# Optimization experiments

Hardware: AMD Instinct MI355X
Metric: run time of the kernel (lower is better)

The kernel has to match this reference:

```python
import jax, jax.numpy as jnp
import numpy as np

# --- constants from config ---
CU, CV, F, BASE = 257.446, 197.718, 387.777, 0.239965
INLIER_THRESHOLD = 0.5
ERROR_TOLERANCE = 0.5   # '3D'
NUM_ITERATIONS = 256
DIM = '3D'
BATCH, NPTS, NSAMP = 64, 16384, 6


def se3_inv(T):
    # T: ...x4x4 SE(3); inverse = [R^T, -R^T t]
    R = T[..., :3, :3]
    t = T[..., :3, 3:4]
    Rt = jnp.swapaxes(R, -1, -2)
    top = jnp.concatenate([Rt, -Rt @ t], axis=-1)
    bottom = jnp.broadcast_to(jnp.array([0.0, 0.0, 0.0, 1.0], T.dtype), top.shape[:-2] + (1, 4))
    return jnp.concatenate([top, bottom], axis=-2)


def weighted_svd_transform(src, trg, w):
    # src, trg: Bx4xS homogeneous points; w: Bx1xS weights. Returns T_trg_src (Bx4x4).
    ps, pt = src[:, :3, :], trg[:, :3, :]
    w_sum = jnp.sum(w, axis=2, keepdims=True)
    cs = jnp.sum(ps * w, axis=2, keepdims=True) / w_sum  # Bx3x1
    ct = jnp.sum(pt * w, axis=2, keepdims=True) / w_sum
    qs, qt = ps - cs, pt - ct
    cov = jnp.einsum('bis,bjs->bij', qt * w, qs)  # Bx3x3
    U, _, Vt = jnp.linalg.svd(cov)
    det = jnp.linalg.det(U @ Vt)
    diag = jnp.stack([jnp.ones_like(det), jnp.ones_like(det), det], axis=-1)  # Bx3
    R = jnp.einsum('bij,bj,bjk->bik', U, diag, Vt)
    t = ct - R @ cs
    top = jnp.concatenate([R, t], axis=2)
    bottom = jnp.broadcast_to(jnp.array([0.0, 0.0, 0.0, 1.0], src.dtype), (src.shape[0], 1, 4))
    return jnp.concatenate([top, bottom], axis=1)


def stereo_project(pts):
    # pts: Bx4xN homogeneous camera-frame points -> Bx4xN stereo image coords (ul, vl, ur, vr)
    M = jnp.array([[F, 0.0, CU, 0.0],
                   [0.0, F, CV, 0.0],
                   [F, 0.0, CU, -F * BASE],
                   [0.0, F, CV, 0.0]], pts.dtype)
    z = pts[:, 2:3, :]
    return jnp.einsum('ij,bjn->bin', M, pts) / z


def setup_inputs() -> dict:
    key = jax.random.key(0)
    ks = jax.random.split(key, 6)
    def homog(k):
        p = jax.random.normal(k, (BATCH, 3, NPTS), jnp.float32) * 5.0
        p = p.at[:, 2, :].set(jnp.abs(p[:, 2, :]) + 1.0)  # positive depth
        return jnp.concatenate([p, jnp.ones((BATCH, 1, NPTS), jnp.float32)], axis=1)
    keypoints_3D_src = homog(ks[0])
    keypoints_3D_trg = homog(ks[1])
    keypoints_2D_trg = jax.random.uniform(ks[2], (BATCH, 2, NPTS), jnp.float32) * 512.0
    valid_pts_src = jax.random.randint(ks[3], (BATCH, 1, NPTS), 0, 2).astype(jnp.int32)
    valid_pts_trg = jax.random.randint(ks[4], (BATCH, 1, NPTS), 0, 2).astype(jnp.int32)
    weights = jax.random.uniform(ks[5], (BATCH, 1, NPTS), jnp.float32, 1e-3, 1.0)
    # vehicle->sensor transform: small rotation about x + translation
    c, s = np.cos(0.1), np.sin(0.1)
    T_s_v = jnp.array([[1, 0, 0, 0.2], [0, c, -s, 0.0], [0, s, c, 1.0], [0, 0, 0, 1]], jnp.float32)
    return {'keypoints_3D_src': keypoints_3D_src, 'keypoints_3D_trg': keypoints_3D_trg,
            'keypoints_2D_trg': keypoints_2D_trg, 'valid_pts_src': valid_pts_src,
            'valid_pts_trg': valid_pts_trg, 'weights': weights, 'T_s_v': T_s_v}


def reference(keypoints_3D_src, keypoints_3D_trg, keypoints_2D_trg,
              valid_pts_src, valid_pts_trg, weights, T_s_v):
    B, _, N = keypoints_3D_src.shape
    pts_src = jax.lax.stop_gradient(keypoints_3D_src)
    pts_trg = jax.lax.stop_gradient(keypoints_3D_trg)
    pts2_trg = jax.lax.stop_gradient(keypoints_2D_trg)
    w = jax.lax.stop_gradient(weights)
    valid = (valid_pts_src[:, 0, :] > 0) & (valid_pts_trg[:, 0, :] > 0)  # BxN
    T_s_v_b = jnp.broadcast_to(T_s_v, (B, 4, 4))
    T_v_s_b = se3_inv(T_s_v_b)

    rand_idx = jax.random.randint(jax.random.key(42), (NUM_ITERATIONS, B, NSAMP), 0, N)

    def body(carry, idx):
        max_inl, inliers = carry
        idx4 = idx[:, None, :]
        s_src = jnp.take_along_axis(pts_src, jnp.broadcast_to(idx4, (B, 4, NSAMP)), axis=2)
        s_trg = jnp.take_along_axis(pts_trg, jnp.broadcast_to(idx4, (B, 4, NSAMP)), axis=2)
        s_w = jnp.take_along_axis(w, idx4, axis=2)
        T_trg_src = weighted_svd_transform(s_src, s_trg, s_w)          # Bx4x4
        T_cam = T_s_v_b @ T_trg_src @ T_v_s_b                          # Bx4x4
        est_3D = jnp.einsum('bij,bjn->bin', T_cam, pts_src)            # Bx4xN
        if DIM == '2D':
            est_2D = stereo_project(est_3D)[:, 0:2, :]
            err = jnp.linalg.norm(pts2_trg - est_2D, axis=1)
        else:
            err = jnp.linalg.norm(pts_trg[:, 0:3, :] - est_3D[:, 0:3, :], axis=1)
        small = (err < ERROR_TOLERANCE) & valid                        # BxN
        num = jnp.sum(small, axis=1).astype(jnp.int32)                 # B
        better = num > max_inl
        inliers = jnp.where(better[:, None], small, inliers)
        max_inl = jnp.where(better, num, max_inl)
        return (max_inl, inliers), None

    init = (jnp.zeros((B,), jnp.int32), jnp.zeros((B, N), bool))
    (_, inliers), _ = jax.lax.scan(body, init, rand_idx)
    return inliers.astype(jnp.float32)
```

## Files before the change

### kernel.cpp

```cpp
#include <hip/hip_runtime.h>
#include <stdint.h>
#include <math.h>

#define NPTS   16384
#define NBATCH 64
#define NITER  256
#define NSAMP  6
#define PPT    16
#define NCHUNK 4
#define ISPLIT 8
#define IPB    (NITER / ISPLIT)

__device__ __forceinline__ uint32_t rotl32(uint32_t v, uint32_t r) {
  return (v << r) | (v >> (32u - r));
}
__device__ __forceinline__ void tf_round(uint32_t& x0, uint32_t& x1, uint32_t r) {
  x0 += x1; x1 = rotl32(x1, r); x1 ^= x0;
}
__device__ void threefry2x32(uint32_t k0, uint32_t k1, uint32_t x0, uint32_t x1,
                             uint32_t& o0, uint32_t& o1) {
  uint32_t ks2 = k0 ^ k1 ^ 0x1BD11BDAu;
  x0 += k0; x1 += k1;
  tf_round(x0,x1,13); tf_round(x0,x1,15); tf_round(x0,x1,26); tf_round(x0,x1,6);
  x0 += k1; x1 += ks2 + 1u;
  tf_round(x0,x1,17); tf_round(x0,x1,29); tf_round(x0,x1,16); tf_round(x0,x1,24);
  x0 += ks2; x1 += k0 + 2u;
  tf_round(x0,x1,13); tf_round(x0,x1,15); tf_round(x0,x1,26); tf_round(x0,x1,6);
  x0 += k0; x1 += k1 + 3u;
  tf_round(x0,x1,17); tf_round(x0,x1,29); tf_round(x0,x1,16); tf_round(x0,x1,24);
  x0 += k1; x1 += ks2 + 4u;
  tf_round(x0,x1,13); tf_round(x0,x1,15); tf_round(x0,x1,26); tf_round(x0,x1,6);
  x0 += ks2; x1 += k0 + 5u;
  o0 = x0; o1 = x1;
}

template<int P, int Q>
__device__ __forceinline__ void jrot(double S[3][3], double V[3][3]) {
  double apq = S[P][Q];
  if (fabs(apq) > 1e-300) {
    double tau = (S[Q][Q] - S[P][P]) / (2.0 * apq);
    double t = copysign(1.0, tau) / (fabs(tau) + sqrt(1.0 + tau * tau));
    double c = 1.0 / sqrt(1.0 + t * t);
    double sn = t * c;
    #pragma unroll
    for (int k = 0; k < 3; ++k) {
      double skp = S[k][P], skq = S[k][Q];
      S[k][P] = c * skp - sn * skq;
      S[k][Q] = sn * skp + c * skq;
    }
    #pragma unroll
    for (int k = 0; k < 3; ++k) {
      double spk = S[P][k], sqk = S[Q][k];
      S[P][k] = c * spk - sn * sqk;
      S[Q][k] = sn * spk + c * sqk;
    }
    #pragma unroll
    for (int k = 0; k < 3; ++k) {
      double vkp = V[k][P], vkq = V[k][Q];
      V[k][P] = c * vkp - sn * vkq;
      V[k][Q] = sn * vkp + c * vkq;
    }
  }
}

__device__ __forceinline__ void swapd(double& a, double& b) { double t=a; a=b; b=t; }

__global__ __launch_bounds__(64) void fit_kernel(
    const float* __restrict__ src, const float* __restrict__ trg,
    const float* __restrict__ wts, const float* __restrict__ Tsv,
    float* __restrict__ models ,
    int* __restrict__ counts ) {
  const int b = blockIdx.x >> 2;
  const int iter = ((blockIdx.x & 3) << 6) | threadIdx.x;

  counts[b * NITER + iter] = 0;

  uint32_t K0, K1;
  threefry2x32(0u, 42u, 0u, 1u, K0, K1);

  const uint32_t base = (uint32_t)((iter * NBATCH + b) * NSAMP);
  int idx[NSAMP];
  #pragma unroll
  for (int s = 0; s < NSAMP; ++s) {
    uint32_t y0, y1;
    threefry2x32(K0, K1, 0u, base + (uint32_t)s, y0, y1);
    idx[s] = (int)((y0 ^ y1) & (uint32_t)(NPTS - 1));
  }

  const float* sb = src + (size_t)b * 4 * NPTS;
  const float* tb = trg + (size_t)b * 4 * NPTS;
  const float* wb = wts + (size_t)b * NPTS;

  float px[NSAMP], py[NSAMP], pz[NSAMP], qx[NSAMP], qy[NSAMP], qz[NSAMP], wv[NSAMP];
  #pragma unroll
  for (int s = 0; s < NSAMP; ++s) {
    int j = idx[s];
    px[s] = sb[j]; py[s] = sb[NPTS + j]; pz[s] = sb[2 * NPTS + j];
    qx[s] = tb[j]; qy[s] = tb[NPTS + j]; qz[s] = tb[2 * NPTS + j];
    wv[s] = wb[j];
  }

  double wsum = 0, csx = 0, csy = 0, csz = 0, ctx = 0, cty = 0, ctz = 0;
  #pragma unroll
  for (int s = 0; s < NSAMP; ++s) {
    double w = (double)wv[s];
    wsum += w;
    csx += (double)px[s] * w; csy += (double)py[s] * w; csz += (double)pz[s] * w;
    ctx += (double)qx[s] * w; cty += (double)qy[s] * w; ctz += (double)qz[s] * w;
  }
  double iw = 1.0 / wsum;
  csx *= iw; csy *= iw; csz *= iw; ctx *= iw; cty *= iw; ctz *= iw;

  double C00=0,C01=0,C02=0,C10=0,C11=0,C12=0,C20=0,C21=0,C22=0;
  #pragma unroll
  for (int s = 0; s < NSAMP; ++s) {
    double w = (double)wv[s];
    double ax = ((double)qx[s]-ctx)*w, ay = ((double)qy[s]-cty)*w, az = ((double)qz[s]-ctz)*w;
    double bx = (double)px[s]-csx, by = (double)py[s]-csy, bz = (double)pz[s]-csz;
    C00 += ax*bx; C01 += ax*by; C02 += ax*bz;
    C10 += ay*bx; C11 += ay*by; C12 += ay*bz;
    C20 += az*bx; C21 += az*by; C22 += az*bz;
  }

  double S[3][3], V[3][3] = {{1,0,0},{0,1,0},{0,0,1}};
  S[0][0] = C00*C00 + C10*C10 + C20*C20;
  S[0][1] = C00*C01 + C10*C11 + C20*C21;
  S[0][2] = C00*C02 + C10*C12 + C20*C22;
  S[1][1] = C01*C01 + C11*C11 + C21*C21;
  S[1][2] = C01*C02 + C11*C12 + C21*C22;
  S[2][2] = C02*C02 + C12*C12 + C22*C22;
  S[1][0] = S[0][1]; S[2][0] = S[0][2]; S[2][1] = S[1][2];
  #pragma unroll 1
  for (int sweep = 0; sweep < 6; ++sweep) {
    jrot<0,1>(S, V); jrot<0,2>(S, V); jrot<1,2>(S, V);
  }

  double l0 = S[0][0], l1 = S[1][1], l2 = S[2][2];
  double v0x=V[0][0], v0y=V[1][0], v0z=V[2][0];
  double v1x=V[0][1], v1y=V[1][1], v1z=V[2][1];
  double v2x=V[0][2], v2y=V[1][2], v2z=V[2][2];
  if (l0 < l1) { swapd(l0,l1); swapd(v0x,v1x); swapd(v0y,v1y); swapd(v0z,v1z); }
  if (l1 < l2) { swapd(l1,l2); swapd(v1x,v2x); swapd(v1y,v2y); swapd(v1z,v2z); }
  if (l0 < l1) { swapd(l0,l1); swapd(v0x,v1x); swapd(v0y,v1y); swapd(v0z,v1z); }

  double u0x = C00*v0x + C01*v0y + C02*v0z;
  double u0y = C10*v0x + C11*v0y + C12*v0z;
  double u0z = C20*v0x + C21*v0y + C22*v0z;
  double n0 = sqrt(u0x*u0x + u0y*u0y + u0z*u0z);
  double r0 = (n0 > 1e-150) ? 1.0 / n0 : 0.0;
  u0x *= r0; u0y *= r0; u0z *= r0;
  double u1x = C00*v1x + C01*v1y + C02*v1z;
  double u1y = C10*v1x + C11*v1y + C12*v1z;
  double u1z = C20*v1x + C21*v1y + C22*v1z;
  double d01 = u1x*u0x + u1y*u0y + u1z*u0z;
  u1x -= d01*u0x; u1y -= d01*u0y; u1z -= d01*u0z;
  double n1 = sqrt(u1x*u1x + u1y*u1y + u1z*u1z);
  double r1 = (n1 > 1e-150) ? 1.0 / n1 : 0.0;
  u1x *= r1; u1y *= r1; u1z *= r1;
  double u2x = u0y*u1z - u0z*u1y;
  double u2y = u0z*u1x - u0x*u1z;
  double u2z = u0x*u1y - u0y*u1x;
  double detV = v0x*(v1y*v2z - v1z*v2y) - v0y*(v1x*v2z - v1z*v2x) + v0z*(v1x*v2y - v1y*v2x);
  double R00 = u0x*v0x + u1x*v1x + detV*u2x*v2x;
  double R01 = u0x*v0y + u1x*v1y + detV*u2x*v2y;
  double R02 = u0x*v0z + u1x*v1z + detV*u2x*v2z;
  double R10 = u0y*v0x + u1y*v1x + detV*u2y*v2x;
  double R11 = u0y*v0y + u1y*v1y + detV*u2y*v2y;
  double R12 = u0y*v0z + u1y*v1z + detV*u2y*v2z;
  double R20 = u0z*v0x + u1z*v1x + detV*u2z*v2x;
  double R21 = u0z*v0y + u1z*v1y + detV*u2z*v2y;
  double R22 = u0z*v0z + u1z*v1z + detV*u2z*v2z;
  double tx = ctx - (R00*csx + R01*csy + R02*csz);
  double ty = cty - (R10*csx + R11*csy + R12*csz);
  double tz = ctz - (R20*csx + R21*csy + R22*csz);

  double A[4][4];
  #pragma unroll
  for (int i = 0; i < 4; ++i)
    #pragma unroll
    for (int j = 0; j < 4; ++j) A[i][j] = (double)Tsv[i*4 + j];
  double Tts[4][4] = {{R00,R01,R02,tx},{R10,R11,R12,ty},{R20,R21,R22,tz},{0,0,0,1}};
  double I[4][4];
  I[0][0]=A[0][0]; I[0][1]=A[1][0]; I[0][2]=A[2][0];
  I[1][0]=A[0][1]; I[1][1]=A[1][1]; I[1][2]=A[2][1];
  I[2][0]=A[0][2]; I[2][1]=A[1][2]; I[2][2]=A[2][2];
  I[0][3] = -(I[0][0]*A[0][3] + I[0][1]*A[1][3] + I[0][2]*A[2][3]);
  I[1][3] = -(I[1][0]*A[0][3] + I[1][1]*A[1][3] + I[1][2]*A[2][3]);
  I[2][3] = -(I[2][0]*A[0][3] + I[2][1]*A[1][3] + I[2][2]*A[2][3]);
  I[3][0]=0; I[3][1]=0; I[3][2]=0; I[3][3]=1;
  double M1[4][4];
  #pragma unroll
  for (int i = 0; i < 4; ++i)
    #pragma unroll
    for (int j = 0; j < 4; ++j)
      M1[i][j] = A[i][0]*Tts[0][j] + A[i][1]*Tts[1][j] + A[i][2]*Tts[2][j] + A[i][3]*Tts[3][j];
  float* mo = models + ((size_t)b * NITER + iter) * 12;
  #pragma unroll
  for (int i = 0; i < 3; ++i)
    #pragma unroll
    for (int j = 0; j < 4; ++j)
      mo[i*4 + j] = (float)(M1[i][0]*I[0][j] + M1[i][1]*I[1][j] + M1[i][2]*I[2][j] + M1[i][3]*I[3][j]);
}

__global__ __launch_bounds__(256) void count_kernel(
    const float* __restrict__ src, const float* __restrict__ trg,
    const int* __restrict__ vs, const int* __restrict__ vt,
    const float* __restrict__ models, int* __restrict__ counts) {
  __shared__ float4 M4[IPB * 3];
  __shared__ int cl[IPB];
  const int b      = blockIdx.x >> 5;
  const int isplit = (blockIdx.x >> 2) & (ISPLIT - 1);
  const int chunk  = blockIdx.x & (NCHUNK - 1);
  const int ibase  = isplit * IPB;

  const float4* mb4 = (const float4*)(models + ((size_t)b * NITER + ibase) * 12);
  for (int i = threadIdx.x; i < IPB * 3; i += 256) M4[i] = mb4[i];
  if (threadIdx.x < IPB) cl[threadIdx.x] = 0;
  __syncthreads();

  const float* sb = src + (size_t)b * 4 * NPTS;
  const float* tb = trg + (size_t)b * 4 * NPTS;
  const int* vsb = vs + (size_t)b * NPTS;
  const int* vtb = vt + (size_t)b * NPTS;
  const int p0 = chunk * (256 * PPT) + threadIdx.x;

  float sx[PPT], sy[PPT], sz[PPT], tx[PPT], ty[PPT], tz[PPT];
  #pragma unroll
  for (int k = 0; k < PPT; ++k) {
    int p = p0 + k * 256;
    bool vd = (vsb[p] > 0) && (vtb[p] > 0);
    sx[k] = sb[p]; sy[k] = sb[NPTS + p]; sz[k] = sb[2 * NPTS + p];
    tx[k] = vd ? tb[p] : 3.0e38f;
    ty[k] = tb[NPTS + p]; tz[k] = tb[2 * NPTS + p];
  }

  for (int it = 0; it < IPB; it += 2) {
    float4 r0 = M4[it * 3 + 0], r1 = M4[it * 3 + 1], r2 = M4[it * 3 + 2];
    int c0 = 0;
    #pragma unroll
    for (int k = 0; k < PPT; ++k) {
      float ex = fmaf(r0.x, sx[k], fmaf(r0.y, sy[k], fmaf(r0.z, sz[k], r0.w)));
      float ey = fmaf(r1.x, sx[k], fmaf(r1.y, sy[k], fmaf(r1.z, sz[k], r1.w)));
      float ez = fmaf(r2.x, sx[k], fmaf(r2.y, sy[k], fmaf(r2.z, sz[k], r2.w)));
      float dx = tx[k] - ex, dy = ty[k] - ey, dz = tz[k] - ez;
      float e2 = fmaf(dx, dx, fmaf(dy, dy, dz * dz));
      c0 += (e2 < 0.25f) ? 1 : 0;
    }
    float4 q0 = M4[it * 3 + 3], q1 = M4[it * 3 + 4], q2 = M4[it * 3 + 5];
    int c1 = 0;
    #pragma unroll
    for (int k = 0; k < PPT; ++k) {
      float ex = fmaf(q0.x, sx[k], fmaf(q0.y, sy[k], fmaf(q0.z, sz[k], q0.w)));
      float ey = fmaf(q1.x, sx[k], fmaf(q1.y, sy[k], fmaf(q1.z, sz[k], q1.w)));
      float ez = fmaf(q2.x, sx[k], fmaf(q2.y, sy[k], fmaf(q2.z, sz[k], q2.w)));
      float dx = tx[k] - ex, dy = ty[k] - ey, dz = tz[k] - ez;
      float e2 = fmaf(dx, dx, fmaf(dy, dy, dz * dz));
      c1 += (e2 < 0.25f) ? 1 : 0;
    }
    unsigned s = (unsigned)c0 | ((unsigned)c1 << 16);
    s += __shfl_xor(s, 32); s += __shfl_xor(s, 16); s += __shfl_xor(s, 8);
    s += __shfl_xor(s, 4);  s += __shfl_xor(s, 2);  s += __shfl_xor(s, 1);
    const int lane = threadIdx.x & 63;
    if (lane == 0)      atomicAdd(&cl[it],     (int)(s & 0xffffu));
    else if (lane == 1) atomicAdd(&cl[it + 1], (int)(s >> 16));
  }
  __syncthreads();
  if (threadIdx.x < IPB)
    atomicAdd(&counts[(size_t)b * NITER + ibase + threadIdx.x], cl[threadIdx.x]);
}

__global__ __launch_bounds__(256) void output_kernel(
    const float* __restrict__ src, const float* __restrict__ trg,
    const int* __restrict__ vs, const int* __restrict__ vt,
    const float* __restrict__ models, const int* __restrict__ counts,
    float* __restrict__ out) {
  const int tid = blockIdx.x * 256 + threadIdx.x;
  const int b = tid >> 14;
  const int p = tid & (NPTS - 1);

  __shared__ int sbest[4];
  {
    int c = counts[b * NITER + threadIdx.x];
    int key = (c << 8) | (NITER - 1 - threadIdx.x);
    key = max(key, __shfl_xor(key, 32));
    key = max(key, __shfl_xor(key, 16));
    key = max(key, __shfl_xor(key, 8));
    key = max(key, __shfl_xor(key, 4));
    key = max(key, __shfl_xor(key, 2));
    key = max(key, __shfl_xor(key, 1));
    if ((threadIdx.x & 63) == 0) sbest[threadIdx.x >> 6] = key;
  }
  __syncthreads();
  const int best = max(max(sbest[0], sbest[1]), max(sbest[2], sbest[3]));
  const int it = (NITER - 1) - (best & 255);

  const float* m = models + ((size_t)b * NITER + it) * 12;
  float m00=m[0], m01=m[1], m02=m[2],  m03=m[3];
  float m10=m[4], m11=m[5], m12=m[6],  m13=m[7];
  float m20=m[8], m21=m[9], m22=m[10], m23=m[11];
  const float* sb = src + (size_t)b * 4 * NPTS;
  const float* tb = trg + (size_t)b * 4 * NPTS;
  float sxv = sb[p], syv = sb[NPTS + p], szv = sb[2 * NPTS + p];
  float txv = tb[p], tyv = tb[NPTS + p], tzv = tb[2 * NPTS + p];
  bool v = (vs[(size_t)b * NPTS + p] > 0) && (vt[(size_t)b * NPTS + p] > 0);
  float ex = fmaf(m00, sxv, fmaf(m01, syv, fmaf(m02, szv, m03)));
  float ey = fmaf(m10, sxv, fmaf(m11, syv, fmaf(m12, szv, m13)));
  float ez = fmaf(m20, sxv, fmaf(m21, syv, fmaf(m22, szv, m23)));
  float dx = txv - ex, dy = tyv - ey, dz = tzv - ez;
  float e2 = fmaf(dx, dx, fmaf(dy, dy, dz * dz));
  out[tid] = (e2 < 0.25f && v) ? 1.0f : 0.0f;
}

extern "C" void kernel_launch(void* const* d_in, const int* in_sizes, int n_in,
                              void* d_out, int out_size, void* d_ws, size_t ws_size,
                              hipStream_t stream) {
  (void)in_sizes; (void)n_in; (void)out_size; (void)ws_size;
  const float* src = (const float*)d_in[0];
  const float* trg = (const float*)d_in[1];
  const int*   vs  = (const int*)d_in[3];
  const int*   vt  = (const int*)d_in[4];
  const float* wts = (const float*)d_in[5];
  const float* Tsv = (const float*)d_in[6];
  float* out = (float*)d_out;

  char* ws = (char*)d_ws;
  float* models = (float*)ws;
  int* counts   = (int*)(ws + (size_t)NBATCH * NITER * 12 * 4);

  fit_kernel<<<NBATCH * 4, 64, 0, stream>>>(src, trg, wts, Tsv, models, counts);
  count_kernel<<<NBATCH * ISPLIT * NCHUNK, 256, 0, stream>>>(src, trg, vs, vt, models, counts);
  output_kernel<<<(NBATCH * NPTS) / 256, 256, 0, stream>>>(src, trg, vs, vt, models, counts, out);
}
```

Measured before the change: 216.9 us.

## Vectorize point loads, read models via scalar loads, drop shared-memory staging in count kernel

The count kernel now gives each thread a contiguous run of 16 points and loads them with float4/int4 vector loads instead of strided scalar loads. Model matrices are read straight from global memory as wave-uniform values (likely scalar loads) instead of being staged in LDS behind a barrier. Per-wave counts go straight to global atomics instead of block-local LDS atomics, and launch bounds now request 3 blocks per SIMD. This trades LDS traffic and the barrier for more global atomics and a possible rise in register pressure.

```diff
diff --git a/kernel.cpp b/kernel.cpp
--- a/kernel.cpp
+++ b/kernel.cpp
@@ -202,57 +202,68 @@
       mo[i*4 + j] = (float)(M1[i][0]*I[0][j] + M1[i][1]*I[1][j] + M1[i][2]*I[2][j] + M1[i][3]*I[3][j]);
 }
 
-__global__ __launch_bounds__(256) void count_kernel(
+__global__ __launch_bounds__(256, 3) void count_kernel(
     const float* __restrict__ src, const float* __restrict__ trg,
     const int* __restrict__ vs, const int* __restrict__ vt,
     const float* __restrict__ models, int* __restrict__ counts) {
-  __shared__ float4 M4[IPB * 3];
-  __shared__ int cl[IPB];
   const int b      = blockIdx.x >> 5;
   const int isplit = (blockIdx.x >> 2) & (ISPLIT - 1);
   const int chunk  = blockIdx.x & (NCHUNK - 1);
   const int ibase  = isplit * IPB;
 
-  const float4* mb4 = (const float4*)(models + ((size_t)b * NITER + ibase) * 12);
-  for (int i = threadIdx.x; i < IPB * 3; i += 256) M4[i] = mb4[i];
-  if (threadIdx.x < IPB) cl[threadIdx.x] = 0;
-  __syncthreads();
-
   const float* sb = src + (size_t)b * 4 * NPTS;
   const float* tb = trg + (size_t)b * 4 * NPTS;
   const int* vsb = vs + (size_t)b * NPTS;
   const int* vtb = vt + (size_t)b * NPTS;
-  const int p0 = chunk * (256 * PPT) + threadIdx.x;
+  const int p0 = chunk * (256 * PPT) + threadIdx.x * PPT;
 
   float sx[PPT], sy[PPT], sz[PPT], tx[PPT], ty[PPT], tz[PPT];
   #pragma unroll
-  for (int k = 0; k < PPT; ++k) {
-    int p = p0 + k * 256;
-    bool vd = (vsb[p] > 0) && (vtb[p] > 0);
-    sx[k] = sb[p]; sy[k] = sb[NPTS + p]; sz[k] = sb[2 * NPTS + p];
-    tx[k] = vd ? tb[p] : 3.0e38f;
-    ty[k] = tb[NPTS + p]; tz[k] = tb[2 * NPTS + p];
-  }
-
+  for (int q = 0; q < PPT / 4; ++q) {
+    float4 a = *(const float4*)(sb + p0 + 4 * q);
+    float4 c = *(const float4*)(sb + NPTS + p0 + 4 * q);
+    float4 d = *(const float4*)(sb + 2 * NPTS + p0 + 4 * q);
+    float4 e = *(const float4*)(tb + p0 + 4 * q);
+    float4 f = *(const float4*)(tb + NPTS + p0 + 4 * q);
+    float4 g = *(const float4*)(tb + 2 * NPTS + p0 + 4 * q);
+    int4 va = *(const int4*)(vsb + p0 + 4 * q);
+    int4 vb = *(const int4*)(vtb + p0 + 4 * q);
+    sx[4*q+0]=a.x; sx[4*q+1]=a.y; sx[4*q+2]=a.z; sx[4*q+3]=a.w;
+    sy[4*q+0]=c.x; sy[4*q+1]=c.y; sy[4*q+2]=c.z; sy[4*q+3]=c.w;
+    sz[4*q+0]=d.x; sz[4*q+1]=d.y; sz[4*q+2]=d.z; sz[4*q+3]=d.w;
+    tx[4*q+0] = (va.x>0 && vb.x>0) ? e.x : 3.0e38f;
+    tx[4*q+1] = (va.y>0 && vb.y>0) ? e.y : 3.0e38f;
+    tx[4*q+2] = (va.z>0 && vb.z>0) ? e.z : 3.0e38f;
+    tx[4*q+3] = (va.w>0 && vb.w>0) ? e.w : 3.0e38f;
+    ty[4*q+0]=f.x; ty[4*q+1]=f.y; ty[4*q+2]=f.z; ty[4*q+3]=f.w;
+    tz[4*q+0]=g.x; tz[4*q+1]=g.y; tz[4*q+2]=g.z; tz[4*q+3]=g.w;
+  }
+
+  const float* mp = models + ((size_t)b * NITER + ibase) * 12;
+  #pragma unroll 1
   for (int it = 0; it < IPB; it += 2) {
-    float4 r0 = M4[it * 3 + 0], r1 = M4[it * 3 + 1], r2 = M4[it * 3 + 2];
-    int c0 = 0;
+    const float* m = mp + it * 12;
+    float m00=m[0],  m01=m[1],  m02=m[2],  m03=m[3];
+    float m10=m[4],  m11=m[5],  m12=m[6],  m13=m[7];
+    float m20=m[8],  m21=m[9],  m22=m[10], m23=m[11];
+    float n00=m[12], n01=m[13], n02=m[14], n03=m[15];
+    float n10=m[16], n11=m[17], n12=m[18], n13=m[19];
+    float n20=m[20], n21=m[21], n22=m[22], n23=m[23];
+    int c0 = 0, c1 = 0;
     #pragma unroll
     for (int k = 0; k < PPT; ++k) {
-      float ex = fmaf(r0.x, sx[k], fmaf(r0.y, sy[k], fmaf(r0.z, sz[k], r0.w)));
-      float ey = fmaf(r1.x, sx[k], fmaf(r1.y, sy[k], fmaf(r1.z, sz[k], r1.w)));
-      float ez = fmaf(r2.x, sx[k], fmaf(r2.y, sy[k], fmaf(r2.z, sz[k], r2.w)));
+      float ex = fmaf(m00, sx[k], fmaf(m01, sy[k], fmaf(m02, sz[k], m03)));
+      float ey = fmaf(m10, sx[k], fmaf(m11, sy[k], fmaf(m12, sz[k], m13)));
+      float ez = fmaf(m20, sx[k], fmaf(m21, sy[k], fmaf(m22, sz[k], m23)));
       float dx = tx[k] - ex, dy = ty[k] - ey, dz = tz[k] - ez;
       float e2 = fmaf(dx, dx, fmaf(dy, dy, dz * dz));
       c0 += (e2 < 0.25f) ? 1 : 0;
     }
-    float4 q0 = M4[it * 3 + 3], q1 = M4[it * 3 + 4], q2 = M4[it * 3 + 5];
-    int c1 = 0;
     #pragma unroll
     for (int k = 0; k < PPT; ++k) {
-      float ex = fmaf(q0.x, sx[k], fmaf(q0.y, sy[k], fmaf(q0.z, sz[k], q0.w)));
-      float ey = fmaf(q1.x, sx[k], fmaf(q1.y, sy[k], fmaf(q1.z, sz[k], q1.w)));
-      float ez = fmaf(q2.x, sx[k], fmaf(q2.y, sy[k], fmaf(q2.z, sz[k], q2.w)));
+      float ex = fmaf(n00, sx[k], fmaf(n01, sy[k], fmaf(n02, sz[k], n03)));
+      float ey = fmaf(n10, sx[k], fmaf(n11, sy[k], fmaf(n12, sz[k], n13)));
+      float ez = fmaf(n20, sx[k], fmaf(n21, sy[k], fmaf(n22, sz[k], n23)));
       float dx = tx[k] - ex, dy = ty[k] - ey, dz = tz[k] - ez;
       float e2 = fmaf(dx, dx, fmaf(dy, dy, dz * dz));
       c1 += (e2 < 0.25f) ? 1 : 0;
@@ -261,12 +272,9 @@
     s += __shfl_xor(s, 32); s += __shfl_xor(s, 16); s += __shfl_xor(s, 8);
     s += __shfl_xor(s, 4);  s += __shfl_xor(s, 2);  s += __shfl_xor(s, 1);
     const int lane = threadIdx.x & 63;
-    if (lane == 0)      atomicAdd(&cl[it],     (int)(s & 0xffffu));
-    else if (lane == 1) atomicAdd(&cl[it + 1], (int)(s >> 16));
-  }
-  __syncthreads();
-  if (threadIdx.x < IPB)
-    atomicAdd(&counts[(size_t)b * NITER + ibase + threadIdx.x], cl[threadIdx.x]);
+    if (lane == 0)      atomicAdd(&counts[(size_t)b * NITER + ibase + it],     (int)(s & 0xffffu));
+    else if (lane == 1) atomicAdd(&counts[(size_t)b * NITER + ibase + it + 1], (int)(s >> 16));
+  }
 }
 
 __global__ __launch_bounds__(256) void output_kernel(
```

Measured after the change: 204.4 us. -5.8%, faster.
